# Optimization experiments

Hardware: AMD Instinct MI355X
Metric: run time of the kernel (lower is better)

The kernel has to match this reference:

```python
import jax, jax.numpy as jnp
import numpy as np

TAU = 0.5  # temperature
W_SCALE = 1.0 / np.sqrt(2048.0)  # keep logits in a sane range (like nn.Linear init)


def setup_inputs() -> dict:
    key = jax.random.key(0)
    k1, k2, k3 = jax.random.split(key, 3)
    B, I, O, N = 8192, 2048, 256, 64
    x = jax.random.normal(k1, (B, I), dtype=jnp.float32)
    W = jax.random.normal(k2, (O, N, I), dtype=jnp.float32) * W_SCALE
    b = jnp.zeros((O, N), dtype=jnp.float32)
    grid = jnp.linspace(-1.0, 1.0, N, dtype=jnp.float32)
    # pre-sampled standard Gumbel noise (reparameterized sampling, fixed for determinism)
    u = jax.random.uniform(k3, (B, O, N), dtype=jnp.float32, minval=1e-6, maxval=1.0 - 1e-6)
    gumbel_noise = -jnp.log(-jnp.log(u))
    return {"x": x, "W": W, "b": b, "grid": grid, "gumbel_noise": gumbel_noise}


def reference(x, W, b, grid, gumbel_noise):
    B = x.shape[0]
    O, N, _ = W.shape
    # per-output-feature linears fused into one GEMM; stack(dim=-1) order -> [B, N, O]
    factors = jnp.einsum('bi,oni->bno', x, W) + b.T  # [B, n_bins, out_features]
    # torch .view(B, out_features, n_bins) on the contiguous stacked tensor == reshape
    factors_logits = factors.reshape(B, O, N)
    # gumbel-softmax sampling (soft), then collapse bins onto the value grid
    y = jax.nn.softmax((factors_logits + gumbel_noise) / TAU, axis=-1)  # [B, O, N]
    encoded = jnp.einsum('bon,n->bo', y, grid)  # [B, out_features]
    return (encoded, factors_logits)
```

## Files before the change

### kernel.cpp

```cpp
#include <hip/hip_runtime.h>
#include <hip/hip_bf16.h>
#include <stdint.h>

typedef __bf16 bf16x8 __attribute__((ext_vector_type(8)));
typedef float f32x4 __attribute__((ext_vector_type(4)));
typedef unsigned short u16x8 __attribute__((ext_vector_type(8)));

#define B_ROWS 8192
#define K_DIM  2048
#define O_DIM  256
#define N_BINS 64
#define J_DIM  (O_DIM * N_BINS)

__device__ __forceinline__ unsigned short f2bf(float f) {
    union { float f; unsigned u; } v; v.f = f;
    unsigned r = (v.u + 0x7fffu + ((v.u >> 16) & 1u)) >> 16;
    return (unsigned short)r;
}

__global__ void cvt_x_kernel(const float* __restrict__ x, unsigned short* __restrict__ xb) {
    int i = (blockIdx.x * 256 + threadIdx.x) * 4;
    float4 v = *(const float4*)(x + i);
    ushort4 o;
    o.x = f2bf(v.x); o.y = f2bf(v.y); o.z = f2bf(v.z); o.w = f2bf(v.w);
    *(ushort4*)(xb + i) = o;
}

__global__ void cvt_w_kernel(const float* __restrict__ W, unsigned short* __restrict__ vb) {
    int bid = blockIdx.x;
    int p   = bid >> 1;
    int i0  = (bid & 1) * 1024 + threadIdx.x * 4;
    int src = (p & (O_DIM - 1)) * (N_BINS * K_DIM) + (p >> 8) * K_DIM + i0;
    float4 v = *(const float4*)(W + src);
    ushort4 o;
    o.x = f2bf(v.x); o.y = f2bf(v.y); o.z = f2bf(v.z); o.w = f2bf(v.w);
    *(ushort4*)(vb + (size_t)p * K_DIM + i0) = o;
}

__device__ __forceinline__ u16x8 pack8(float4 a, float4 b) {
    u16x8 r;
    r[0] = f2bf(a.x); r[1] = f2bf(a.y); r[2] = f2bf(a.z); r[3] = f2bf(a.w);
    r[4] = f2bf(b.x); r[5] = f2bf(b.y); r[6] = f2bf(b.z); r[7] = f2bf(b.w);
    return r;
}

#define GLDS(gsrc, ldst) \
    __builtin_amdgcn_global_load_lds((const __attribute__((address_space(1))) void*)(gsrc), \
                                     (__attribute__((address_space(3))) void*)(ldst), 16, 0, 0)
#define SBAR()   __builtin_amdgcn_s_barrier()
#define WAIT_VM(N) do { asm volatile("s_waitcnt vmcnt(" #N ")" ::: "memory"); } while (0)
#define MFMA(a, b, c) (c) = __builtin_amdgcn_mfma_f32_16x16x32_bf16((a), (b), (c), 0, 0, 0)

#define KTILE_BODY(BUF, STAGE_A, STAGE_B) do {                                          \
    bf16x8 a0_[2], a1_[2], bf_[4];                                                      \
    _Pragma("unroll") for (int n_ = 0; n_ < 4; ++n_)                                    \
        bf_[n_] = *(const bf16x8*)&Bs[BUF][brb + n_ * 16][slot];                        \
    _Pragma("unroll") for (int m_ = 0; m_ < 2; ++m_)                                    \
        a0_[m_] = *(const bf16x8*)&As[BUF][arb + m_ * 16][slot];                        \
    STAGE_A;                                                                            \
    __builtin_amdgcn_s_setprio(1);                                                      \
    _Pragma("unroll") for (int m_ = 0; m_ < 2; ++m_) {                                  \
        MFMA(a0_[m_], bf_[0], acc[m_][0]); MFMA(a0_[m_], bf_[1], acc[m_][1]);           \
        MFMA(a0_[m_], bf_[2], acc[m_][2]); MFMA(a0_[m_], bf_[3], acc[m_][3]);           \
    }                                                                                   \
    __builtin_amdgcn_s_setprio(0);                                                      \
    _Pragma("unroll") for (int m_ = 0; m_ < 2; ++m_)                                    \
        a1_[m_] = *(const bf16x8*)&As[BUF][arb + 32 + m_ * 16][slot];                   \
    STAGE_B;                                                                            \
    __builtin_amdgcn_s_setprio(1);                                                      \
    _Pragma("unroll") for (int m_ = 0; m_ < 2; ++m_) {                                  \
        MFMA(a1_[m_], bf_[0], acc[2 + m_][0]); MFMA(a1_[m_], bf_[1], acc[2 + m_][1]);   \
        MFMA(a1_[m_], bf_[2], acc[2 + m_][2]); MFMA(a1_[m_], bf_[3], acc[2 + m_][3]);   \
    }                                                                                   \
    __builtin_amdgcn_s_setprio(0);                                                      \
} while (0)

__global__ __launch_bounds__(1024, 4) void gemm8_kernel(
    const unsigned short* __restrict__ xb,
    const unsigned short* __restrict__ vb,
    const float* __restrict__ bias,
    const float* __restrict__ grid,
    const float* __restrict__ gumbel,
    float* __restrict__ logits,
    float* __restrict__ encoded)
{
    __shared__ __align__(16) unsigned char pool[131072];
    auto As = (unsigned short (*)[256][32])pool;
    auto Bs = (unsigned short (*)[256][32])(pool + 65536);
    float* ep = (float*)pool;

    const int tid  = threadIdx.x;
    const int lane = tid & 63;
    const int wv   = tid >> 6;
    const int wr   = wv >> 2;
    const int wc   = wv & 3;

    const int bid = blockIdx.x;
    const int swz  = (bid & 7) * 256 + (bid >> 3);
    const int bm   = (swz >> 8) * 4 + (swz & 3);
    const int bn   = (swz & 255) >> 2;
    const int row0 = bm * 256;
    const int col0 = bn * 256;

    const int oss = (tid * 16) ^ (tid & 32);
    const int sr  = oss >> 6;
    const int sc  = (oss >> 1) & 31;

    const unsigned short* gA = xb + (size_t)(row0 + sr) * K_DIM + sc;
    const unsigned short* gB = vb + (size_t)(col0 + sr) * K_DIM + sc;

    auto stageA = [&](int k, int b) {
        GLDS(gA + k * 32, &As[b][0][0] + wv * 512);
    };
    auto stageB = [&](int k, int b) {
        GLDS(gB + k * 32, &Bs[b][0][0] + wv * 512);
    };

    const int arb  = wr * 64 + (lane & 15);
    const int brb  = wc * 64 + (lane & 15);
    const int slot = ((lane >> 4) * 8) ^ ((lane & 8) << 1);

    f32x4 acc[4][4];
#pragma unroll
    for (int m = 0; m < 4; ++m)
#pragma unroll
        for (int n = 0; n < 4; ++n)
            acc[m][n] = (f32x4){0.f, 0.f, 0.f, 0.f};

    stageA(0, 0); stageB(0, 0);
    stageA(1, 1); stageB(1, 1);
    stageA(2, 2); stageB(2, 2);

    for (int it = 0; it < 15; ++it) {
        const int kt0 = it * 4;
#pragma unroll
        for (int u = 0; u < 4; ++u) {
            WAIT_VM(4); SBAR();
            KTILE_BODY(u, stageA(kt0 + u + 3, (u + 3) & 3), stageB(kt0 + u + 3, (u + 3) & 3));
        }
    }
    WAIT_VM(4); SBAR(); KTILE_BODY(0, stageA(63, 3), stageB(63, 3));
    WAIT_VM(4); SBAR(); KTILE_BODY(1, (void)0, (void)0);
    WAIT_VM(2); SBAR(); KTILE_BODY(2, (void)0, (void)0);
    WAIT_VM(0); SBAR(); KTILE_BODY(3, (void)0, (void)0);

    SBAR();

    const int lane15 = lane & 15;
    const int hi4    = lane >> 4;

    float biasv[4];
#pragma unroll
    for (int n = 0; n < 4; ++n) {
        const int c = col0 + wc * 64 + n * 16 + lane15;
        biasv[n] = bias[(c & (O_DIM - 1)) * N_BINS + (c >> 8)];
    }
    const float4 gridv = *(const float4*)(grid + lane15 * 4);

#pragma unroll
    for (int h = 0; h < 2; ++h) {
        if ((wr >> 1) == h) {
#pragma unroll
            for (int m = 0; m < 4; ++m)
#pragma unroll
                for (int n = 0; n < 4; ++n) {
                    const int cd = wc * 64 + n * 16 + lane15;
#pragma unroll
                    for (int q = 0; q < 4; ++q) {
                        const int rl = (wr & 1) * 64 + m * 16 + hi4 * 4 + q;
                        ep[rl * 256 + (cd ^ ((rl & 7) << 2))] = acc[m][n][q] + biasv[n];
                    }
                }
        }
        SBAR();

        const int cb = hi4 * 64 + lane15 * 4;
        const float* gptr = gumbel + (size_t)(row0 + h * 128 + wv) * J_DIM + col0 + cb;
        float*       lptr = logits + (size_t)(row0 + h * 128 + wv) * J_DIM + col0 + cb;

        float4 gq[4];
#pragma unroll
        for (int p = 0; p < 4; ++p)
            gq[p] = *(const float4*)(gptr + (size_t)p * 16 * J_DIM);

#pragma unroll
        for (int i = 0; i < 8; ++i) {
            const int r = i * 16 + wv;
            const float4 L = *(const float4*)&ep[r * 256 + (cb ^ ((r & 7) << 2))];
            const float4 G = gq[i & 3];
            if (i < 4)
                gq[i & 3] = *(const float4*)(gptr + (size_t)(i + 4) * 16 * J_DIM);

            float z0 = (L.x + G.x) * 2.0f;
            float z1 = (L.y + G.y) * 2.0f;
            float z2 = (L.z + G.z) * 2.0f;
            float z3 = (L.w + G.w) * 2.0f;
            float gmax = fmaxf(fmaxf(z0, z1), fmaxf(z2, z3));
#pragma unroll
            for (int s = 1; s < 16; s <<= 1) gmax = fmaxf(gmax, __shfl_xor(gmax, s));

            const float e0 = __expf(z0 - gmax), e1 = __expf(z1 - gmax);
            const float e2 = __expf(z2 - gmax), e3 = __expf(z3 - gmax);
            float ss = e0 + e1 + e2 + e3;
            float ds = e0 * gridv.x + e1 * gridv.y + e2 * gridv.z + e3 * gridv.w;
#pragma unroll
            for (int s = 1; s < 16; s <<= 1) {
                ss += __shfl_xor(ss, s);
                ds += __shfl_xor(ds, s);
            }

            *(float4*)(lptr + (size_t)i * 16 * J_DIM) = L;
            if (lane15 == 0)
                encoded[(size_t)(row0 + h * 128 + r) * O_DIM + (col0 >> 6) + hi4] = ds / ss;
        }
        SBAR();
    }
}

__global__ __launch_bounds__(256) void gemm_fb(
    const float* __restrict__ xf,
    const float* __restrict__ Wf,
    const float* __restrict__ bias,
    float* __restrict__ logits)
{
    __shared__ unsigned short Asm_[128 * 32];
    __shared__ unsigned short Bsm_[128 * 32];

    const int tid = threadIdx.x;
    const int bid = blockIdx.x;
    const int swz = (bid & 7) * 1024 + (bid >> 3);
    const int row0 = (swz >> 7) * 128;
    const int col0 = (swz & 127) * 128;

    const int lane = tid & 63;
    const int wid  = tid >> 6;
    const int wr   = wid >> 1;
    const int wc   = wid & 1;

    f32x4 acc[4][4];
#pragma unroll
    for (int m = 0; m < 4; ++m)
#pragma unroll
        for (int n = 0; n < 4; ++n)
            acc[m][n] = (f32x4){0.f, 0.f, 0.f, 0.f};

    const int srow = tid >> 2;
    const int koff = (tid & 3) * 8;
    const int ra0 = row0 + srow, ra1 = row0 + 64 + srow;
    const int rb0 = col0 + srow, rb1 = col0 + 64 + srow;

    unsigned short* la0 = &Asm_[tid * 8];
    unsigned short* la1 = &Asm_[(256 + tid) * 8];
    unsigned short* lb0 = &Bsm_[tid * 8];
    unsigned short* lb1 = &Bsm_[(256 + tid) * 8];

    const float* fa0 = xf + (size_t)ra0 * K_DIM + koff;
    const float* fa1 = xf + (size_t)ra1 * K_DIM + koff;
    const float* fb0 = Wf + (size_t)((rb0 & (O_DIM - 1)) * (N_BINS * K_DIM) + (rb0 >> 8) * K_DIM) + koff;
    const float* fb1 = Wf + (size_t)((rb1 & (O_DIM - 1)) * (N_BINS * K_DIM) + (rb1 >> 8) * K_DIM) + koff;

    const int a_row  = wr * 64 + (lane & 15);
    const int b_row  = wc * 64 + (lane & 15);
    const int k_half = (lane >> 4) * 8;

    for (int kt = 0; kt < K_DIM / 32; ++kt) {
        const int kbase = kt * 32;
        *(u16x8*)la0 = pack8(*(const float4*)(fa0 + kbase), *(const float4*)(fa0 + kbase + 4));
        *(u16x8*)la1 = pack8(*(const float4*)(fa1 + kbase), *(const float4*)(fa1 + kbase + 4));
        *(u16x8*)lb0 = pack8(*(const float4*)(fb0 + kbase), *(const float4*)(fb0 + kbase + 4));
        *(u16x8*)lb1 = pack8(*(const float4*)(fb1 + kbase), *(const float4*)(fb1 + kbase + 4));
        __syncthreads();
        bf16x8 af[4], bg[4];
#pragma unroll
        for (int m = 0; m < 4; ++m) af[m] = *(const bf16x8*)&Asm_[(a_row + m * 16) * 32 + k_half];
#pragma unroll
        for (int n = 0; n < 4; ++n) bg[n] = *(const bf16x8*)&Bsm_[(b_row + n * 16) * 32 + k_half];
#pragma unroll
        for (int m = 0; m < 4; ++m)
#pragma unroll
            for (int n = 0; n < 4; ++n)
                MFMA(af[m], bg[n], acc[m][n]);
        __syncthreads();
    }

    const int r_base = row0 + wr * 64 + (lane >> 4) * 4;
    const int c_base = col0 + wc * 64 + (lane & 15);
#pragma unroll
    for (int n = 0; n < 4; ++n) {
        const int c = c_base + n * 16;
        const float bv = bias[(c & (O_DIM - 1)) * N_BINS + (c >> 8)];
#pragma unroll
        for (int m = 0; m < 4; ++m) {
            const int r = r_base + m * 16;
            float* out = logits + (size_t)r * J_DIM + c;
#pragma unroll
            for (int q = 0; q < 4; ++q)
                out[(size_t)q * J_DIM] = acc[m][n][q] + bv;
        }
    }
}

__global__ void softmax_encode_kernel(
    const float* __restrict__ logits,
    const float* __restrict__ gumbel,
    const float* __restrict__ grid,
    float* __restrict__ encoded)
{
    int t = blockIdx.x * 256 + threadIdx.x;
    int g = t >> 4;
    int l = t & 15;
    size_t base = (size_t)g * 64 + l * 4;
    float4 L = *(const float4*)(logits + base);
    float4 G = *(const float4*)(gumbel + base);
    float4 gr = *(const float4*)(grid + l * 4);

    float z0 = (L.x + G.x) * 2.0f;
    float z1 = (L.y + G.y) * 2.0f;
    float z2 = (L.z + G.z) * 2.0f;
    float z3 = (L.w + G.w) * 2.0f;

    float m = fmaxf(fmaxf(z0, z1), fmaxf(z2, z3));
#pragma unroll
    for (int s = 1; s < 16; s <<= 1) m = fmaxf(m, __shfl_xor(m, s, 16));

    float e0 = __expf(z0 - m), e1 = __expf(z1 - m), e2 = __expf(z2 - m), e3 = __expf(z3 - m);
    float ssum = e0 + e1 + e2 + e3;
    float dsum = e0 * gr.x + e1 * gr.y + e2 * gr.z + e3 * gr.w;
#pragma unroll
    for (int s = 1; s < 16; s <<= 1) {
        ssum += __shfl_xor(ssum, s, 16);
        dsum += __shfl_xor(dsum, s, 16);
    }
    if (l == 0) encoded[g] = dsum / ssum;
}

extern "C" void kernel_launch(void* const* d_in, const int* in_sizes, int n_in,
                              void* d_out, int out_size, void* d_ws, size_t ws_size,
                              hipStream_t stream) {
    const float* x      = (const float*)d_in[0];
    const float* W      = (const float*)d_in[1];
    const float* bias   = (const float*)d_in[2];
    const float* grid   = (const float*)d_in[3];
    const float* gumbel = (const float*)d_in[4];

    float* encoded = (float*)d_out;
    float* logits  = (float*)d_out + (size_t)B_ROWS * O_DIM;

    const size_t xb_bytes = (size_t)B_ROWS * K_DIM * 2;
    const size_t vb_bytes = (size_t)J_DIM * K_DIM * 2;

    if (ws_size >= xb_bytes + vb_bytes) {
        unsigned short* xb = (unsigned short*)d_ws;
        unsigned short* vb = (unsigned short*)((char*)d_ws + xb_bytes);
        cvt_x_kernel<<<(B_ROWS * K_DIM) / 1024, 256, 0, stream>>>(x, xb);
        cvt_w_kernel<<<J_DIM * 2, 256, 0, stream>>>(W, vb);
        gemm8_kernel<<<(B_ROWS / 256) * (J_DIM / 256), 1024, 0, stream>>>(
            xb, vb, bias, grid, gumbel, logits, encoded);
    } else {
        gemm_fb<<<(B_ROWS / 128) * (J_DIM / 128), 256, 0, stream>>>(x, W, bias, logits);
        softmax_encode_kernel<<<(B_ROWS * O_DIM * 16) / 256, 256, 0, stream>>>(logits, gumbel, grid, encoded);
    }
}
```

Baseline: 781.0 us.

## Shrink GEMM tile to 256x128 with 512 threads and double-buffered LDS

Changes the fused GEMM+gumbel-softmax kernel from 256x256 tiles with 1024 threads and a 4-stage LDS pipeline to 256x128 tiles with 512 threads and a 2-stage double buffer, halving LDS to 64KB. The goal is to let more workgroups reside per CU and raise occupancy. The epilogue is remapped so each wave handles two rows. The cost is a shallower prefetch, since every k-tile now waits on vmcnt(0), and lower operand reuse per loaded byte of x.

```diff
diff --git a/kernel.cpp b/kernel.cpp
--- a/kernel.cpp
+++ b/kernel.cpp
@@ -51,31 +51,33 @@
 #define WAIT_VM(N) do { asm volatile("s_waitcnt vmcnt(" #N ")" ::: "memory"); } while (0)
 #define MFMA(a, b, c) (c) = __builtin_amdgcn_mfma_f32_16x16x32_bf16((a), (b), (c), 0, 0, 0)
 
-#define KTILE_BODY(BUF, STAGE_A, STAGE_B) do {                                          \
-    bf16x8 a0_[2], a1_[2], bf_[4];                                                      \
+#define KTILE(BUF, STAGE_A, STAGE_B, VMW) do {                                          \
+    bf16x8 af_[4], bg_[4];                                                              \
     _Pragma("unroll") for (int n_ = 0; n_ < 4; ++n_)                                    \
-        bf_[n_] = *(const bf16x8*)&Bs[BUF][brb + n_ * 16][slot];                        \
+        bg_[n_] = *(const bf16x8*)&Bs[BUF][brb + n_ * 16][slot];                        \
     _Pragma("unroll") for (int m_ = 0; m_ < 2; ++m_)                                    \
-        a0_[m_] = *(const bf16x8*)&As[BUF][arb + m_ * 16][slot];                        \
+        af_[m_] = *(const bf16x8*)&As[BUF][arb + m_ * 16][slot];                        \
     STAGE_A;                                                                            \
     __builtin_amdgcn_s_setprio(1);                                                      \
     _Pragma("unroll") for (int m_ = 0; m_ < 2; ++m_) {                                  \
-        MFMA(a0_[m_], bf_[0], acc[m_][0]); MFMA(a0_[m_], bf_[1], acc[m_][1]);           \
-        MFMA(a0_[m_], bf_[2], acc[m_][2]); MFMA(a0_[m_], bf_[3], acc[m_][3]);           \
+        MFMA(af_[m_], bg_[0], acc[m_][0]); MFMA(af_[m_], bg_[1], acc[m_][1]);           \
+        MFMA(af_[m_], bg_[2], acc[m_][2]); MFMA(af_[m_], bg_[3], acc[m_][3]);           \
     }                                                                                   \
     __builtin_amdgcn_s_setprio(0);                                                      \
-    _Pragma("unroll") for (int m_ = 0; m_ < 2; ++m_)                                    \
-        a1_[m_] = *(const bf16x8*)&As[BUF][arb + 32 + m_ * 16][slot];                   \
+    _Pragma("unroll") for (int m_ = 2; m_ < 4; ++m_)                                    \
+        af_[m_] = *(const bf16x8*)&As[BUF][arb + m_ * 16][slot];                        \
     STAGE_B;                                                                            \
     __builtin_amdgcn_s_setprio(1);                                                      \
-    _Pragma("unroll") for (int m_ = 0; m_ < 2; ++m_) {                                  \
-        MFMA(a1_[m_], bf_[0], acc[2 + m_][0]); MFMA(a1_[m_], bf_[1], acc[2 + m_][1]);   \
-        MFMA(a1_[m_], bf_[2], acc[2 + m_][2]); MFMA(a1_[m_], bf_[3], acc[2 + m_][3]);   \
+    _Pragma("unroll") for (int m_ = 2; m_ < 4; ++m_) {                                  \
+        MFMA(af_[m_], bg_[0], acc[m_][0]); MFMA(af_[m_], bg_[1], acc[m_][1]);           \
+        MFMA(af_[m_], bg_[2], acc[m_][2]); MFMA(af_[m_], bg_[3], acc[m_][3]);           \
     }                                                                                   \
     __builtin_amdgcn_s_setprio(0);                                                      \
+    VMW;                                                                                \
+    SBAR();                                                                             \
 } while (0)
 
-__global__ __launch_bounds__(1024, 4) void gemm8_kernel(
+__global__ __launch_bounds__(512, 4) void gemm8_kernel(
     const unsigned short* __restrict__ xb,
     const unsigned short* __restrict__ vb,
     const float* __restrict__ bias,
@@ -84,23 +86,23 @@
     float* __restrict__ logits,
     float* __restrict__ encoded)
 {
-    __shared__ __align__(16) unsigned char pool[131072];
+    __shared__ __align__(16) unsigned char pool[65536];
     auto As = (unsigned short (*)[256][32])pool;
-    auto Bs = (unsigned short (*)[256][32])(pool + 65536);
+    auto Bs = (unsigned short (*)[128][32])(pool + 32768);
     float* ep = (float*)pool;
 
     const int tid  = threadIdx.x;
     const int lane = tid & 63;
     const int wv   = tid >> 6;
-    const int wr   = wv >> 2;
-    const int wc   = wv & 3;
+    const int wr   = wv >> 1;
+    const int wc   = wv & 1;
 
     const int bid = blockIdx.x;
-    const int swz  = (bid & 7) * 256 + (bid >> 3);
-    const int bm   = (swz >> 8) * 4 + (swz & 3);
-    const int bn   = (swz & 255) >> 2;
+    const int swz  = (bid & 7) * 512 + (bid >> 3);
+    const int bm   = (swz >> 9) * 4 + (swz & 3);
+    const int bn   = (swz & 511) >> 2;
     const int row0 = bm * 256;
-    const int col0 = bn * 256;
+    const int col0 = bn * 128;
 
     const int oss = (tid * 16) ^ (tid & 32);
     const int sr  = oss >> 6;
@@ -110,7 +112,10 @@
     const unsigned short* gB = vb + (size_t)(col0 + sr) * K_DIM + sc;
 
     auto stageA = [&](int k, int b) {
-        GLDS(gA + k * 32, &As[b][0][0] + wv * 512);
+        const unsigned short* g = gA + k * 32;
+        unsigned short* l = &As[b][0][0] + wv * 512;
+        GLDS(g, l);
+        GLDS(g + (size_t)128 * K_DIM, l + 4096);
     };
     auto stageB = [&](int k, int b) {
         GLDS(gB + k * 32, &Bs[b][0][0] + wv * 512);
@@ -128,21 +133,15 @@
             acc[m][n] = (f32x4){0.f, 0.f, 0.f, 0.f};
 
     stageA(0, 0); stageB(0, 0);
-    stageA(1, 1); stageB(1, 1);
-    stageA(2, 2); stageB(2, 2);
-
-    for (int it = 0; it < 15; ++it) {
-        const int kt0 = it * 4;
-#pragma unroll
-        for (int u = 0; u < 4; ++u) {
-            WAIT_VM(4); SBAR();
-            KTILE_BODY(u, stageA(kt0 + u + 3, (u + 3) & 3), stageB(kt0 + u + 3, (u + 3) & 3));
-        }
-    }
-    WAIT_VM(4); SBAR(); KTILE_BODY(0, stageA(63, 3), stageB(63, 3));
-    WAIT_VM(4); SBAR(); KTILE_BODY(1, (void)0, (void)0);
-    WAIT_VM(2); SBAR(); KTILE_BODY(2, (void)0, (void)0);
-    WAIT_VM(0); SBAR(); KTILE_BODY(3, (void)0, (void)0);
+    WAIT_VM(0); SBAR();
+
+    for (int it = 0; it < 31; ++it) {
+        const int k2 = it * 2;
+        KTILE(0, stageA(k2 + 1, 1), stageB(k2 + 1, 1), WAIT_VM(0));
+        KTILE(1, stageA(k2 + 2, 0), stageB(k2 + 2, 0), WAIT_VM(0));
+    }
+    KTILE(0, stageA(63, 1), stageB(63, 1), WAIT_VM(0));
+    KTILE(1, (void)0, (void)0, (void)0);
 
     SBAR();
 
@@ -157,6 +156,9 @@
     }
     const float4 gridv = *(const float4*)(grid + lane15 * 4);
 
+    const int rofs = lane >> 5;
+    const int cb   = (lane & 31) * 4;
+
 #pragma unroll
     for (int h = 0; h < 2; ++h) {
         if ((wr >> 1) == h) {
@@ -168,28 +170,24 @@
 #pragma unroll
                     for (int q = 0; q < 4; ++q) {
                         const int rl = (wr & 1) * 64 + m * 16 + hi4 * 4 + q;
-                        ep[rl * 256 + (cd ^ ((rl & 7) << 2))] = acc[m][n][q] + biasv[n];
+                        ep[rl * 128 + (cd ^ ((rl & 7) << 2))] = acc[m][n][q] + biasv[n];
                     }
                 }
         }
         SBAR();
 
-        const int cb = hi4 * 64 + lane15 * 4;
-        const float* gptr = gumbel + (size_t)(row0 + h * 128 + wv) * J_DIM + col0 + cb;
-        float*       lptr = logits + (size_t)(row0 + h * 128 + wv) * J_DIM + col0 + cb;
-
-        float4 gq[4];
-#pragma unroll
-        for (int p = 0; p < 4; ++p)
-            gq[p] = *(const float4*)(gptr + (size_t)p * 16 * J_DIM);
-
+        const size_t rbase = (size_t)(row0 + h * 128 + wv * 2 + rofs);
+        const float* gptr = gumbel + rbase * J_DIM + col0 + cb;
+        float*       lptr = logits + rbase * J_DIM + col0 + cb;
+
+        float4 gq = *(const float4*)(gptr);
 #pragma unroll
         for (int i = 0; i < 8; ++i) {
-            const int r = i * 16 + wv;
-            const float4 L = *(const float4*)&ep[r * 256 + (cb ^ ((r & 7) << 2))];
-            const float4 G = gq[i & 3];
-            if (i < 4)
-                gq[i & 3] = *(const float4*)(gptr + (size_t)(i + 4) * 16 * J_DIM);
+            const int r = i * 16 + wv * 2 + rofs;
+            const float4 L = *(const float4*)&ep[r * 128 + (cb ^ ((r & 7) << 2))];
+            const float4 G = gq;
+            if (i < 7)
+                gq = *(const float4*)(gptr + (size_t)(i + 1) * 16 * J_DIM);
 
             float z0 = (L.x + G.x) * 2.0f;
             float z1 = (L.y + G.y) * 2.0f;
@@ -211,7 +209,7 @@
 
             *(float4*)(lptr + (size_t)i * 16 * J_DIM) = L;
             if (lane15 == 0)
-                encoded[(size_t)(row0 + h * 128 + r) * O_DIM + (col0 >> 6) + hi4] = ds / ss;
+                encoded[(size_t)(row0 + h * 128 + r) * O_DIM + (col0 >> 6) + (hi4 & 1)] = ds / ss;
         }
         SBAR();
     }
@@ -354,7 +352,7 @@
         unsigned short* vb = (unsigned short*)((char*)d_ws + xb_bytes);
         cvt_x_kernel<<<(B_ROWS * K_DIM) / 1024, 256, 0, stream>>>(x, xb);
         cvt_w_kernel<<<J_DIM * 2, 256, 0, stream>>>(W, vb);
-        gemm8_kernel<<<(B_ROWS / 256) * (J_DIM / 256), 1024, 0, stream>>>(
+        gemm8_kernel<<<(B_ROWS / 256) * (J_DIM / 128), 512, 0, stream>>>(
             xb, vb, bias, grid, gumbel, logits, encoded);
     } else {
         gemm_fb<<<(B_ROWS / 128) * (J_DIM / 128), 256, 0, stream>>>(x, W, bias, logits);
```

New measurement: 828.0 us. 6.0% more time.
